# Performance work log

Measured on AMD Instinct MI355X. Metric: run time of the kernel, lower is better.

## Reference

```python
import jax, jax.numpy as jnp
import numpy as np

WS = 8          # window_size
HEADS = 6
DH = 32         # dim_head


def _dwconv(t, w):
    # t: (B,C,H,W), w: (C,1,3,3) depthwise, stride 1, padding 1 -> SAME
    return jax.lax.conv_general_dilated(
        t, w, window_strides=(1, 1), padding='SAME',
        feature_group_count=t.shape[1],
        dimension_numbers=('NCHW', 'OIHW', 'NCHW'))


def _l2norm(t, eps=1e-12):
    # matches F.normalize: x / max(||x||, eps)
    n = jnp.sqrt(jnp.sum(t * t, axis=-1, keepdims=True))
    return t / jnp.maximum(n, eps)


def setup_inputs() -> dict:
    key = jax.random.key(0)
    ks = jax.random.split(key, 10)
    B, H, W, C = 2, 256, 256, 192
    s = 0.05
    return {
        'x': jax.random.normal(ks[0], (B, H, W, C), jnp.float32),
        'illu_fea_trans': jax.random.normal(ks[1], (B, H, W, C), jnp.float32),
        'gt_w': jax.random.normal(ks[2], (C, C), jnp.float32) * s,
        'gt_b': jax.random.normal(ks[3], (C,), jnp.float32) * s,
        'qkv_w': jax.random.normal(ks[4], (C, 3 * C), jnp.float32) * s,
        'qkv_b': jax.random.normal(ks[5], (3 * C,), jnp.float32) * s,
        'proj_w': jax.random.normal(ks[6], (C, C), jnp.float32) * s,
        'proj_b': jax.random.normal(ks[7], (C,), jnp.float32) * s,
        'conv1_w': jax.random.normal(ks[8], (C, 1, 3, 3), jnp.float32) * s,
        'conv2_w': jax.random.normal(ks[9], (C, 1, 3, 3), jnp.float32) * s,
    }


def reference(x, illu_fea_trans, gt_w, gt_b, qkv_w, qkv_b, proj_w, proj_b,
              conv1_w, conv2_w):
    B, H, W, C = x.shape
    Ws, heads, d = WS, HEADS, DH
    scale = d ** (-0.5)
    pad_h = (Ws - H % Ws) % Ws
    pad_w = (Ws - W % Ws) % Ws
    xp = jnp.pad(x, ((0, 0), (0, pad_h), (0, pad_w), (0, 0)), mode='reflect')
    ip = jnp.pad(illu_fea_trans, ((0, 0), (0, pad_h), (0, pad_w), (0, 0)), mode='reflect')
    Hp, Wp = xp.shape[1], xp.shape[2]
    nW = (Hp // Ws) * (Wp // Ws)
    T = Ws * Ws

    def to_windows(t):
        t = t.reshape(B, Hp // Ws, Ws, Wp // Ws, Ws, C)
        return t.transpose(0, 1, 3, 2, 4, 5).reshape(B * nW, T, C)

    xw = to_windows(xp)                                  # (B*nW, T, C)
    qkv = (xw @ qkv_w + qkv_b).reshape(B * nW, T, 3, heads, d)
    qkv = qkv.transpose(2, 0, 3, 1, 4)                   # (3, Bn, h, T, d)
    q, k, v = qkv[0], qkv[1], qkv[2]
    q = _l2norm(q)
    k = _l2norm(k)

    illu = to_windows(ip).reshape(B * nW, T, heads, d).transpose(0, 2, 1, 3)
    v = v * (1.0 + jax.nn.sigmoid(illu))

    # global token: avg-pool over padded spatial dims, then linear
    gt = jnp.mean(xp, axis=(1, 2)) @ gt_w + gt_b          # (B, C)
    gt = gt.reshape(B, heads, 1, d)
    # faithful to torch expand(dim=2 -> nW).reshape(B*nW, heads, 1, d)
    gk = jnp.broadcast_to(gt, (B, heads, nW, d)).reshape(B * nW, heads, 1, d)
    k = jnp.concatenate([k, gk], axis=2)                  # (Bn, h, T+1, d)
    v = jnp.concatenate([v, gk], axis=2)

    # chunked softmax over keys == full softmax over key axis (chunks on q only)
    attn = jax.nn.softmax(jnp.einsum('bhqd,bhkd->bhqk', q, k) * scale, axis=-1)
    out = jnp.einsum('bhqk,bhkd->bhqd', attn, v)          # (Bn, h, T, d)
    out = out.transpose(0, 2, 1, 3).reshape(B * nW, T, C)
    out = out @ proj_w + proj_b

    out = out.reshape(B, Hp // Ws, Wp // Ws, Ws, Ws, C)
    out = out.transpose(0, 1, 3, 2, 4, 5).reshape(B, Hp, Wp, C)[:, :H, :W, :]

    # depthwise-conv positional branch on padded x (exact gelu like torch)
    t = xp.transpose(0, 3, 1, 2)                          # (B,C,Hp,Wp)
    t = _dwconv(t, conv1_w)
    t = jax.nn.gelu(t, approximate=False)
    t = _dwconv(t, conv2_w)
    pos = t.transpose(0, 2, 3, 1)[:, :H, :W, :]
    return out + pos
```

## Files before the change

kernel.cpp:

```cpp
#include <hip/hip_runtime.h>
#include <hip/hip_bf16.h>

#define BB   2
#define HH   256
#define WWD  256
#define CC   192
#define WSZ  8
#define TT   64
#define NHD  6
#define DHD  32
#define N3   576

typedef __attribute__((ext_vector_type(8))) short short8;
typedef __attribute__((ext_vector_type(4))) float f32x4;

__device__ inline short bf16_bits(float f) {
  __hip_bfloat16 h = __float2bfloat16(f);
  return __builtin_bit_cast(short, h);
}

__device__ inline void stage1k(const short* gsrc, short* ldst, int lane) {
  __builtin_amdgcn_global_load_lds(
      (const __attribute__((address_space(1))) void*)(gsrc + lane * 8),
      (__attribute__((address_space(3))) void*)ldst, 16, 0, 0);
}

__global__ __launch_bounds__(256) void lcam_wshuf(const float* __restrict__ src,
                                                  short* __restrict__ dst,
                                                  int ncols, int nfrag, int perm) {
  int gid = blockIdx.x * 256 + threadIdx.x;
  if (gid >= nfrag) return;
  int lane = gid & 63;
  int s = (gid >> 6) % 6;
  int ct = gid / 384;
  int col = ct * 16 + (lane & 15);
  int k0 = s * 32 + (lane >> 4) * 8;
  short8 v;
#pragma unroll
  for (int j = 0; j < 8; ++j)
    v[j] = bf16_bits(src[(size_t)(k0 + j) * ncols + col]);
  int didx = perm ? ((s * (ncols / 16) + ct) * 64 + lane) : gid;
  *(short8*)(dst + (size_t)didx * 8) = v;
}

__global__ __launch_bounds__(256) void lcam_sum_x(const float* __restrict__ x,
                                                  float* __restrict__ sums) {
  int blk = blockIdx.x;
  int b = blk >> 9;
  int chunk = blk & 511;
  const float* xp = x + ((size_t)b * 65536 + (size_t)chunk * 128) * CC;
  int t = threadIdx.x;
  if (t < CC) {
    float acc = 0.f;
    for (int p = 0; p < 128; ++p) acc += xp[(size_t)p * CC + t];
    atomicAdd(&sums[b * CC + t], acc);
  }
}

__global__ void lcam_gt(const float* __restrict__ sums,
                        const float* __restrict__ gt_w,
                        const float* __restrict__ gt_b,
                        float* __restrict__ gt) {
  int b = blockIdx.x;
  int co = threadIdx.x;
  float acc = gt_b[co];
  const float inv = 1.f / 65536.f;
  for (int c = 0; c < CC; ++c)
    acc += sums[b * CC + c] * inv * gt_w[c * CC + co];
  gt[b * CC + co] = acc;
}

__global__ __launch_bounds__(256) void lcam_attn(
    const float* __restrict__ x, const float* __restrict__ illu,
    const short* __restrict__ wf, const short* __restrict__ pwf,
    const float* __restrict__ qkv_b, const float* __restrict__ proj_b,
    const float* __restrict__ gt, float* __restrict__ out) {
  __shared__ __align__(16) short wq[3 * 768 * 8];
  __shared__ __align__(16) short wp[768 * 8];
  __shared__ __align__(16) short ks[65 * 40];
  __shared__ __align__(16) short vt[32 * 72];
  __shared__ __align__(16) short qs[64 * 40];
  __shared__ __align__(16) short ps[64 * 72];

  int w = blockIdx.x;
  int b  = w >> 10;
  int wy = (w >> 5) & 31;
  int wx = w & 31;
  int t  = threadIdx.x;
  int lane = t & 63;
  int rtile = t >> 6;
  int m = lane & 15;
  int quad = lane >> 4;
  int key0 = rtile * 16 + quad * 4;

  size_t base = ((size_t)(b * HH + wy * WSZ) * WWD + wx * WSZ) * CC;

#pragma unroll
  for (int u = 0; u < 9; ++u) {
    int j = rtile * 9 + u;
    int rr = j / 12, ii = j % 12;
    stage1k(wf + (rr * 12) * 3072 + ii * 512, wq + rr * 6144 + ii * 512, lane);
  }

  int apix = rtile * 16 + m;
  size_t arow = base + (size_t)((apix >> 3) * WWD + (apix & 7)) * CC + quad * 8;
  short8 afrag[6];
#pragma unroll
  for (int s = 0; s < 6; ++s) {
    const float* ap = x + arow + s * 32;
    float4 f0 = *(const float4*)(ap);
    float4 f1 = *(const float4*)(ap + 4);
    short8 v;
    v[0] = bf16_bits(f0.x); v[1] = bf16_bits(f0.y);
    v[2] = bf16_bits(f0.z); v[3] = bf16_bits(f0.w);
    v[4] = bf16_bits(f1.x); v[5] = bf16_bits(f1.y);
    v[6] = bf16_bits(f1.z); v[7] = bf16_bits(f1.w);
    afrag[s] = v;
  }
  const short8* wq8 = (const short8*)wq;
  const short8* wp8 = (const short8*)wp;

  f32x4 pacc[12];
#pragma unroll
  for (int ct = 0; ct < 12; ++ct) {
    f32x4 z = {0.f, 0.f, 0.f, 0.f};
    pacc[ct] = z;
  }

  __syncthreads();

  for (int h = 0; h < NHD; ++h) {
#pragma unroll
    for (int u = 0; u < 3; ++u) {
      int ii = rtile * 3 + u;
      stage1k(pwf + h * 6144 + ii * 512, wp + ii * 512, lane);
    }
    float gv0 = gt[b * CC + h * 32 + m];
    float gv1 = gt[b * CC + h * 32 + 16 + m];
    float il0[4], il1[4];
#pragma unroll
    for (int r = 0; r < 4; ++r) {
      int key = key0 + r;
      const float* ip = illu + base + (size_t)((key >> 3) * WWD + (key & 7)) * CC + h * 32;
      il0[r] = ip[m];
      il1[r] = ip[16 + m];
    }
    {
      f32x4 a0 = {0.f,0.f,0.f,0.f}, a1 = {0.f,0.f,0.f,0.f};
      __builtin_amdgcn_s_setprio(1);
#pragma unroll
      for (int s = 0; s < 6; ++s)
        a0 = __builtin_amdgcn_mfma_f32_16x16x32_bf16(afrag[s], wq8[s*64 + lane], a0, 0,0,0);
#pragma unroll
      for (int s = 0; s < 6; ++s)
        a1 = __builtin_amdgcn_mfma_f32_16x16x32_bf16(afrag[s], wq8[384 + s*64 + lane], a1, 0,0,0);
      __builtin_amdgcn_s_setprio(0);
      float b0 = qkv_b[h*32 + m], b1 = qkv_b[h*32 + 16 + m];
#pragma unroll
      for (int r = 0; r < 4; ++r) {
        float v0 = a0[r] + b0, v1 = a1[r] + b1;
        float ss = v0*v0 + v1*v1;
        ss += __shfl_xor(ss, 1); ss += __shfl_xor(ss, 2);
        ss += __shfl_xor(ss, 4); ss += __shfl_xor(ss, 8);
        float scl = 0.17677669529663688f * __builtin_amdgcn_rsqf(fmaxf(ss, 1e-24f));
        int row = key0 + r;
        qs[row*40 + m]      = bf16_bits(v0 * scl);
        qs[row*40 + 16 + m] = bf16_bits(v1 * scl);
      }
    }
    {
      f32x4 a0 = {0.f,0.f,0.f,0.f}, a1 = {0.f,0.f,0.f,0.f};
      __builtin_amdgcn_s_setprio(1);
#pragma unroll
      for (int s = 0; s < 6; ++s)
        a0 = __builtin_amdgcn_mfma_f32_16x16x32_bf16(afrag[s], wq8[768 + s*64 + lane], a0, 0,0,0);
#pragma unroll
      for (int s = 0; s < 6; ++s)
        a1 = __builtin_amdgcn_mfma_f32_16x16x32_bf16(afrag[s], wq8[1152 + s*64 + lane], a1, 0,0,0);
      __builtin_amdgcn_s_setprio(0);
      float b0 = qkv_b[192 + h*32 + m], b1 = qkv_b[192 + h*32 + 16 + m];
#pragma unroll
      for (int r = 0; r < 4; ++r) {
        float v0 = a0[r] + b0, v1 = a1[r] + b1;
        float ss = v0*v0 + v1*v1;
        ss += __shfl_xor(ss, 1); ss += __shfl_xor(ss, 2);
        ss += __shfl_xor(ss, 4); ss += __shfl_xor(ss, 8);
        float scl = __builtin_amdgcn_rsqf(fmaxf(ss, 1e-24f));
        int row = key0 + r;
        ks[row*40 + m]      = bf16_bits(v0 * scl);
        ks[row*40 + 16 + m] = bf16_bits(v1 * scl);
      }
    }
    {
      f32x4 a0 = {0.f,0.f,0.f,0.f}, a1 = {0.f,0.f,0.f,0.f};
      __builtin_amdgcn_s_setprio(1);
#pragma unroll
      for (int s = 0; s < 6; ++s)
        a0 = __builtin_amdgcn_mfma_f32_16x16x32_bf16(afrag[s], wq8[1536 + s*64 + lane], a0, 0,0,0);
#pragma unroll
      for (int s = 0; s < 6; ++s)
        a1 = __builtin_amdgcn_mfma_f32_16x16x32_bf16(afrag[s], wq8[1920 + s*64 + lane], a1, 0,0,0);
      __builtin_amdgcn_s_setprio(0);
      float b0 = qkv_b[384 + h*32 + m], b1 = qkv_b[384 + h*32 + 16 + m];
#pragma unroll
      for (int r = 0; r < 4; ++r) {
        int key = key0 + r;
        float s0 = __builtin_amdgcn_rcpf(1.f + __expf(-il0[r]));
        float s1 = __builtin_amdgcn_rcpf(1.f + __expf(-il1[r]));
        vt[m*72 + key]        = bf16_bits((a0[r] + b0) * (1.f + s0));
        vt[(16 + m)*72 + key] = bf16_bits((a1[r] + b1) * (1.f + s1));
      }
    }
    if (t < DHD) ks[64*40 + t] = bf16_bits(gt[b*CC + h*DHD + t]);
    __syncthreads();
    short8 qa = *(const short8*)(qs + (rtile*16 + m)*40 + quad*8);
    f32x4 sc[5];
#pragma unroll
    for (int ct = 0; ct < 4; ++ct) {
      short8 kb = *(const short8*)(ks + (ct*16 + m)*40 + quad*8);
      f32x4 z = {0.f,0.f,0.f,0.f};
      sc[ct] = __builtin_amdgcn_mfma_f32_16x16x32_bf16(qa, kb, z, 0,0,0);
    }
    {
      short8 kb = *(const short8*)(ks + 64*40 + quad*8);
      f32x4 z = {0.f,0.f,0.f,0.f};
      sc[4] = __builtin_amdgcn_mfma_f32_16x16x32_bf16(qa, kb, z, 0,0,0);
    }
    if (h < NHD - 1) {
#pragma unroll
      for (int u = 0; u < 9; ++u) {
        int j = rtile * 9 + u;
        int rr = j / 12, ii = j % 12;
        stage1k(wf + (rr * 12 + 2 * (h + 1)) * 3072 + ii * 512,
                wq + rr * 6144 + ii * 512, lane);
      }
    }
    float p64v[4], invr[4];
#pragma unroll
    for (int r = 0; r < 4; ++r) {
      float e0 = __expf(sc[0][r]), e1 = __expf(sc[1][r]);
      float e2 = __expf(sc[2][r]), e3 = __expf(sc[3][r]);
      float e4 = (m == 0) ? __expf(sc[4][r]) : 0.f;
      int row = key0 + r;
      ps[row*72 + m]      = bf16_bits(e0);
      ps[row*72 + 16 + m] = bf16_bits(e1);
      ps[row*72 + 32 + m] = bf16_bits(e2);
      ps[row*72 + 48 + m] = bf16_bits(e3);
      float sum = e0 + e1 + e2 + e3 + e4;
      sum += __shfl_xor(sum, 1); sum += __shfl_xor(sum, 2);
      sum += __shfl_xor(sum, 4); sum += __shfl_xor(sum, 8);
      invr[r] = __builtin_amdgcn_rcpf(sum);
      p64v[r] = e4;
    }
    f32x4 o0 = {0.f,0.f,0.f,0.f}, o1 = {0.f,0.f,0.f,0.f};
    __builtin_amdgcn_s_setprio(1);
#pragma unroll
    for (int kc = 0; kc < 2; ++kc) {
      short8 pa  = *(const short8*)(ps + (rtile*16 + m)*72 + kc*32 + quad*8);
      short8 vb0 = *(const short8*)(vt + m*72        + kc*32 + quad*8);
      short8 vb1 = *(const short8*)(vt + (16 + m)*72 + kc*32 + quad*8);
      o0 = __builtin_amdgcn_mfma_f32_16x16x32_bf16(pa, vb0, o0, 0,0,0);
      o1 = __builtin_amdgcn_mfma_f32_16x16x32_bf16(pa, vb1, o1, 0,0,0);
    }
    __builtin_amdgcn_s_setprio(0);
#pragma unroll
    for (int r = 0; r < 4; ++r) {
      float pr = __shfl(p64v[r], lane & 48);
      int row = key0 + r;
      qs[row*40 + m]      = bf16_bits((o0[r] + pr * gv0) * invr[r]);
      qs[row*40 + 16 + m] = bf16_bits((o1[r] + pr * gv1) * invr[r]);
    }
    short8 oa = *(const short8*)(qs + (rtile*16 + m)*40 + quad*8);
    __builtin_amdgcn_s_setprio(1);
#pragma unroll
    for (int ct = 0; ct < 12; ++ct)
      pacc[ct] = __builtin_amdgcn_mfma_f32_16x16x32_bf16(oa, wp8[ct*64 + lane], pacc[ct], 0,0,0);
    __builtin_amdgcn_s_setprio(0);
    __syncthreads();
  }
#pragma unroll
  for (int ct = 0; ct < 12; ++ct) {
    float bias = proj_b[ct*16 + m];
#pragma unroll
    for (int r = 0; r < 4; ++r) {
      int row = key0 + r;
      out[base + (size_t)((row >> 3) * WWD + (row & 7)) * CC + ct*16 + m] = pacc[ct][r] + bias;
    }
  }
}

__global__ __launch_bounds__(256) void lcam_pos(const float* __restrict__ x,
                                                const float* __restrict__ w1,
                                                const float* __restrict__ w2,
                                                float* __restrict__ out) {
  __shared__ __align__(16) float xt[20 * 20 * 16];
  __shared__ float t1[18 * 18 * 16];
  __shared__ float wl1[16 * 9], wl2[16 * 9];
  int blk = blockIdx.x;
  int cgI = blk % 12; int tmp = blk / 12;
  int tx = tmp % 16; tmp /= 16;
  int ty = tmp % 16; int b = tmp / 16;
  int c0 = cgI * 16;
  int y0 = ty * 16, x0 = tx * 16;
  int t = threadIdx.x;
  if (t < 144) { wl1[t] = w1[c0 * 9 + t]; wl2[t] = w2[c0 * 9 + t]; }
  for (int vi = t; vi < 1600; vi += 256) {
    int cc4 = vi & 3;
    int lin = vi >> 2;
    int xx = lin % 20, yy = lin / 20;
    int gy = y0 - 2 + yy, gx = x0 - 2 + xx;
    float4 v = {0.f, 0.f, 0.f, 0.f};
    if (gy >= 0 && gy < HH && gx >= 0 && gx < WWD)
      v = *(const float4*)(x + (((size_t)b * HH + gy) * WWD + gx) * CC + c0 + cc4 * 4);
    *(float4*)(xt + (yy * 20 + xx) * 16 + cc4 * 4) = v;
  }
  __syncthreads();
  for (int idx = t; idx < 5184; idx += 256) {
    int cc = idx & 15;
    int xx = (idx >> 4) % 18;
    int yy = idx / 288;
    int gy = y0 - 1 + yy, gx = x0 - 1 + xx;
    float r = 0.f;
    if (gy >= 0 && gy < HH && gx >= 0 && gx < WWD) {
#pragma unroll
      for (int ky = 0; ky < 3; ++ky)
#pragma unroll
        for (int kx = 0; kx < 3; ++kx)
          r += xt[((yy + ky) * 20 + xx + kx) * 16 + cc] * wl1[cc * 9 + ky * 3 + kx];
      r = 0.5f * r * (1.f + erff(r * 0.70710678118654752f));
    }
    t1[(yy * 18 + xx) * 16 + cc] = r;
  }
  __syncthreads();
  for (int idx = t; idx < 4096; idx += 256) {
    int cc = idx & 15;
    int xx = (idx >> 4) & 15;
    int yy = idx >> 8;
    float r = 0.f;
#pragma unroll
    for (int ky = 0; ky < 3; ++ky)
#pragma unroll
      for (int kx = 0; kx < 3; ++kx)
        r += t1[((yy + ky) * 18 + xx + kx) * 16 + cc] * wl2[cc * 9 + ky * 3 + kx];
    size_t o = (((size_t)b * HH + y0 + yy) * WWD + x0 + xx) * CC + c0 + cc;
    out[o] += r;
  }
}

extern "C" void kernel_launch(void* const* d_in, const int* in_sizes, int n_in,
                              void* d_out, int out_size, void* d_ws, size_t ws_size,
                              hipStream_t stream) {
  const float* x       = (const float*)d_in[0];
  const float* illu    = (const float*)d_in[1];
  const float* gt_w    = (const float*)d_in[2];
  const float* gt_b    = (const float*)d_in[3];
  const float* qkv_w   = (const float*)d_in[4];
  const float* qkv_b   = (const float*)d_in[5];
  const float* proj_w  = (const float*)d_in[6];
  const float* proj_b  = (const float*)d_in[7];
  const float* conv1_w = (const float*)d_in[8];
  const float* conv2_w = (const float*)d_in[9];
  float* out = (float*)d_out;

  short* wf   = (short*)d_ws;
  short* pwf  = (short*)((char*)d_ws + 221184);
  float* sums = (float*)((char*)d_ws + 221184 + 73728);
  float* gt   = sums + BB * CC;

  hipMemsetAsync(sums, 0, BB * CC * sizeof(float), stream);
  lcam_wshuf<<<54, 256, 0, stream>>>(qkv_w, wf, N3, 36 * 6 * 64, 0);
  lcam_wshuf<<<18, 256, 0, stream>>>(proj_w, pwf, CC, 12 * 6 * 64, 1);
  lcam_sum_x<<<1024, 256, 0, stream>>>(x, sums);
  lcam_gt<<<BB, CC, 0, stream>>>(sums, gt_w, gt_b, gt);
  lcam_attn<<<2048, 256, 0, stream>>>(x, illu, wf, pwf, qkv_b, proj_b, gt, out);
  lcam_pos<<<6144, 256, 0, stream>>>(x, conv1_w, conv2_w, out);
}
```

Before: 501.9 us.

## Rotate weight slices through a shared double buffer to cut LDS footprint

Replaces the separate QKV weight buffer (three slices) and projection weight buffer with a two-slot LDS buffer. Each weight slice (Q, K, V, proj) is streamed in just before it is needed, alternating between the two slots. This roughly halves the shared-memory footprint per block, so more blocks can be resident per CU. The cost is two extra block-wide barriers per head and less time to hide the latency of each weight load.

Result: no change. 504.4 us (+0.5%).

```diff
diff --git a/kernel.cpp b/kernel.cpp
--- a/kernel.cpp
+++ b/kernel.cpp
@@ -75,8 +75,7 @@
     const short* __restrict__ wf, const short* __restrict__ pwf,
     const float* __restrict__ qkv_b, const float* __restrict__ proj_b,
     const float* __restrict__ gt, float* __restrict__ out) {
-  __shared__ __align__(16) short wq[3 * 768 * 8];
-  __shared__ __align__(16) short wp[768 * 8];
+  __shared__ __align__(16) short wgt[2][6144];
   __shared__ __align__(16) short ks[65 * 40];
   __shared__ __align__(16) short vt[32 * 72];
   __shared__ __align__(16) short qs[64 * 40];
@@ -96,10 +95,9 @@
   size_t base = ((size_t)(b * HH + wy * WSZ) * WWD + wx * WSZ) * CC;
 
 #pragma unroll
-  for (int u = 0; u < 9; ++u) {
-    int j = rtile * 9 + u;
-    int rr = j / 12, ii = j % 12;
-    stage1k(wf + (rr * 12) * 3072 + ii * 512, wq + rr * 6144 + ii * 512, lane);
+  for (int u = 0; u < 3; ++u) {
+    int ii = rtile * 3 + u;
+    stage1k(wf + ii * 512, wgt[0] + ii * 512, lane);
   }
 
   int apix = rtile * 16 + m;
@@ -117,8 +115,8 @@
     v[6] = bf16_bits(f1.z); v[7] = bf16_bits(f1.w);
     afrag[s] = v;
   }
-  const short8* wq8 = (const short8*)wq;
-  const short8* wp8 = (const short8*)wp;
+  const short8* wA8 = (const short8*)wgt[0];
+  const short8* wB8 = (const short8*)wgt[1];
 
   f32x4 pacc[12];
 #pragma unroll
@@ -133,7 +131,7 @@
 #pragma unroll
     for (int u = 0; u < 3; ++u) {
       int ii = rtile * 3 + u;
-      stage1k(pwf + h * 6144 + ii * 512, wp + ii * 512, lane);
+      stage1k(wf + (12 + 2 * h) * 3072 + ii * 512, wgt[1] + ii * 512, lane);
     }
     float gv0 = gt[b * CC + h * 32 + m];
     float gv1 = gt[b * CC + h * 32 + 16 + m];
@@ -150,10 +148,10 @@
       __builtin_amdgcn_s_setprio(1);
 #pragma unroll
       for (int s = 0; s < 6; ++s)
-        a0 = __builtin_amdgcn_mfma_f32_16x16x32_bf16(afrag[s], wq8[s*64 + lane], a0, 0,0,0);
-#pragma unroll
-      for (int s = 0; s < 6; ++s)
-        a1 = __builtin_amdgcn_mfma_f32_16x16x32_bf16(afrag[s], wq8[384 + s*64 + lane], a1, 0,0,0);
+        a0 = __builtin_amdgcn_mfma_f32_16x16x32_bf16(afrag[s], wA8[s*64 + lane], a0, 0,0,0);
+#pragma unroll
+      for (int s = 0; s < 6; ++s)
+        a1 = __builtin_amdgcn_mfma_f32_16x16x32_bf16(afrag[s], wA8[384 + s*64 + lane], a1, 0,0,0);
       __builtin_amdgcn_s_setprio(0);
       float b0 = qkv_b[h*32 + m], b1 = qkv_b[h*32 + 16 + m];
 #pragma unroll
@@ -168,15 +166,21 @@
         qs[row*40 + 16 + m] = bf16_bits(v1 * scl);
       }
     }
+    __syncthreads();
+#pragma unroll
+    for (int u = 0; u < 3; ++u) {
+      int ii = rtile * 3 + u;
+      stage1k(wf + (24 + 2 * h) * 3072 + ii * 512, wgt[0] + ii * 512, lane);
+    }
     {
       f32x4 a0 = {0.f,0.f,0.f,0.f}, a1 = {0.f,0.f,0.f,0.f};
       __builtin_amdgcn_s_setprio(1);
 #pragma unroll
       for (int s = 0; s < 6; ++s)
-        a0 = __builtin_amdgcn_mfma_f32_16x16x32_bf16(afrag[s], wq8[768 + s*64 + lane], a0, 0,0,0);
-#pragma unroll
-      for (int s = 0; s < 6; ++s)
-        a1 = __builtin_amdgcn_mfma_f32_16x16x32_bf16(afrag[s], wq8[1152 + s*64 + lane], a1, 0,0,0);
+        a0 = __builtin_amdgcn_mfma_f32_16x16x32_bf16(afrag[s], wB8[s*64 + lane], a0, 0,0,0);
+#pragma unroll
+      for (int s = 0; s < 6; ++s)
+        a1 = __builtin_amdgcn_mfma_f32_16x16x32_bf16(afrag[s], wB8[384 + s*64 + lane], a1, 0,0,0);
       __builtin_amdgcn_s_setprio(0);
       float b0 = qkv_b[192 + h*32 + m], b1 = qkv_b[192 + h*32 + 16 + m];
 #pragma unroll
@@ -191,15 +195,21 @@
         ks[row*40 + 16 + m] = bf16_bits(v1 * scl);
       }
     }
+    __syncthreads();
+#pragma unroll
+    for (int u = 0; u < 3; ++u) {
+      int ii = rtile * 3 + u;
+      stage1k(pwf + h * 6144 + ii * 512, wgt[1] + ii * 512, lane);
+    }
     {
       f32x4 a0 = {0.f,0.f,0.f,0.f}, a1 = {0.f,0.f,0.f,0.f};
       __builtin_amdgcn_s_setprio(1);
 #pragma unroll
       for (int s = 0; s < 6; ++s)
-        a0 = __builtin_amdgcn_mfma_f32_16x16x32_bf16(afrag[s], wq8[1536 + s*64 + lane], a0, 0,0,0);
-#pragma unroll
-      for (int s = 0; s < 6; ++s)
-        a1 = __builtin_amdgcn_mfma_f32_16x16x32_bf16(afrag[s], wq8[1920 + s*64 + lane], a1, 0,0,0);
+        a0 = __builtin_amdgcn_mfma_f32_16x16x32_bf16(afrag[s], wA8[s*64 + lane], a0, 0,0,0);
+#pragma unroll
+      for (int s = 0; s < 6; ++s)
+        a1 = __builtin_amdgcn_mfma_f32_16x16x32_bf16(afrag[s], wA8[384 + s*64 + lane], a1, 0,0,0);
       __builtin_amdgcn_s_setprio(0);
       float b0 = qkv_b[384 + h*32 + m], b1 = qkv_b[384 + h*32 + 16 + m];
 #pragma unroll
@@ -213,6 +223,13 @@
     }
     if (t < DHD) ks[64*40 + t] = bf16_bits(gt[b*CC + h*DHD + t]);
     __syncthreads();
+    if (h < NHD - 1) {
+#pragma unroll
+      for (int u = 0; u < 3; ++u) {
+        int ii = rtile * 3 + u;
+        stage1k(wf + 2 * (h + 1) * 3072 + ii * 512, wgt[0] + ii * 512, lane);
+      }
+    }
     short8 qa = *(const short8*)(qs + (rtile*16 + m)*40 + quad*8);
     f32x4 sc[5];
 #pragma unroll
@@ -225,15 +242,6 @@
       short8 kb = *(const short8*)(ks + 64*40 + quad*8);
       f32x4 z = {0.f,0.f,0.f,0.f};
       sc[4] = __builtin_amdgcn_mfma_f32_16x16x32_bf16(qa, kb, z, 0,0,0);
-    }
-    if (h < NHD - 1) {
-#pragma unroll
-      for (int u = 0; u < 9; ++u) {
-        int j = rtile * 9 + u;
-        int rr = j / 12, ii = j % 12;
-        stage1k(wf + (rr * 12 + 2 * (h + 1)) * 3072 + ii * 512,
-                wq + rr * 6144 + ii * 512, lane);
-      }
     }
     float p64v[4], invr[4];
 #pragma unroll
@@ -274,7 +282,7 @@
     __builtin_amdgcn_s_setprio(1);
 #pragma unroll
     for (int ct = 0; ct < 12; ++ct)
-      pacc[ct] = __builtin_amdgcn_mfma_f32_16x16x32_bf16(oa, wp8[ct*64 + lane], pacc[ct], 0,0,0);
+      pacc[ct] = __builtin_amdgcn_mfma_f32_16x16x32_bf16(oa, wB8[ct*64 + lane], pacc[ct], 0,0,0);
     __builtin_amdgcn_s_setprio(0);
     __syncthreads();
   }
```
